# Performance work log

Hardware: AMD Instinct MI355X
Metric: run time of the kernel (lower is better)

Reference implementation:

```python
import jax, jax.numpy as jnp
import numpy as np

B, T, D, U = 32, 2048, 512, 512

def setup_inputs() -> dict:
    key = jax.random.key(0)
    ks = jax.random.split(key, 8)
    s = 0.02
    return {
        "query": jax.random.normal(ks[0], (B, D), dtype=jnp.float32),
        "values": jax.random.normal(ks[1], (B, T, D), dtype=jnp.float32),
        "W1_w": jax.random.normal(ks[2], (D, U), dtype=jnp.float32) * s,
        "W1_b": jnp.zeros((U,), dtype=jnp.float32),
        "W2_w": jax.random.normal(ks[3], (D, U), dtype=jnp.float32) * s,
        "W2_b": jnp.zeros((U,), dtype=jnp.float32),
        "V_w": jax.random.normal(ks[4], (U, 1), dtype=jnp.float32) * s,
        "V_b": jnp.zeros((1,), dtype=jnp.float32),
    }

def reference(query, values, W1_w, W1_b, W2_w, W2_b, V_w, V_b):
    # query: [B, D] -> [B, 1, U]; values: [B, T, D] -> [B, T, U]
    q_proj = (query @ W1_w + W1_b)[:, None, :]              # [B, 1, U]
    v_proj = jnp.einsum('btd,du->btu', values, W2_w) + W2_b  # [B, T, U]
    score = jnp.tanh(q_proj + v_proj) @ V_w + V_b            # [B, T, 1]
    attn = jax.nn.softmax(score, axis=1)                     # [B, T, 1]
    context = jnp.sum(attn * values, axis=1)                 # [B, D]
    return context, attn
```

## Files before the change

### kernel.cpp

```cpp
#include <hip/hip_runtime.h>
#include <hip/hip_bf16.h>
#include <cstddef>
#include <cstdint>

#define B_ 32
#define T_ 2048
#define D_ 512
#define U_ 512

typedef __attribute__((ext_vector_type(8))) short bf16x8;
typedef __attribute__((ext_vector_type(4))) float f32x4;

__device__ __forceinline__ unsigned short f2bf(float f) {
  union { float f; unsigned u; } x; x.f = f;
  unsigned r = x.u + 0x7fffu + ((x.u >> 16) & 1u);
  return (unsigned short)(r >> 16);
}
__device__ __forceinline__ unsigned pack2bf(float a, float b) {
  return (unsigned)f2bf(a) | ((unsigned)f2bf(b) << 16);
}
__device__ __forceinline__ float tanh_fast(float x) {
  float e = __expf(2.0f * x);
  return 1.0f - 2.0f * __builtin_amdgcn_rcpf(e + 1.0f);
}

#define AS1C(p) ((const __attribute__((address_space(1))) unsigned*)(p))
#define AS3(p)  ((__attribute__((address_space(3))) unsigned*)(p))

__global__ void kA_prep(const float* __restrict__ W2, unsigned* __restrict__ W2P,
                        const float* __restrict__ query, const float* __restrict__ W1,
                        const float* __restrict__ W1b, const float* __restrict__ W2b,
                        float* __restrict__ qp, float* __restrict__ score,
                        float* __restrict__ ctx) {
  const int tid = threadIdx.x;
  if (blockIdx.x < 256) {
    #pragma unroll
    for (int ii = 0; ii < 2; ++ii) {
      int p = blockIdx.x * 512 + ii * 256 + tid;
      int j = (p & 3) * 2;
      int l = (p >> 2) & 63;
      int t = p >> 8;
      int u = (t >> 4) * 16 + (l & 15);
      int k = (t & 15) * 32 + ((l >> 4) << 3) + j;
      W2P[p] = pack2bf(W2[(size_t)k * U_ + u], W2[(size_t)(k + 1) * U_ + u]);
    }
  } else {
    __shared__ float qs[D_];
    const int blk = blockIdx.x - 256;
    const int b = blk >> 1, uhh = (blk & 1) * 256;
    qs[tid] = query[b * D_ + tid];
    qs[tid + 256] = query[b * D_ + tid + 256];
    __syncthreads();
    const int u = uhh + tid;
    float a0 = 0, a1 = 0, a2 = 0, a3 = 0, a4 = 0, a5 = 0, a6 = 0, a7 = 0;
    for (int d = 0; d < D_; d += 8) {
      a0 += qs[d + 0] * W1[(size_t)(d + 0) * U_ + u];
      a1 += qs[d + 1] * W1[(size_t)(d + 1) * U_ + u];
      a2 += qs[d + 2] * W1[(size_t)(d + 2) * U_ + u];
      a3 += qs[d + 3] * W1[(size_t)(d + 3) * U_ + u];
      a4 += qs[d + 4] * W1[(size_t)(d + 4) * U_ + u];
      a5 += qs[d + 5] * W1[(size_t)(d + 5) * U_ + u];
      a6 += qs[d + 6] * W1[(size_t)(d + 6) * U_ + u];
      a7 += qs[d + 7] * W1[(size_t)(d + 7) * U_ + u];
    }
    qp[b * U_ + u] = ((a0 + a1) + (a2 + a3)) + ((a4 + a5) + (a6 + a7)) + W1b[u] + W2b[u];
    const int gt = blk * 256 + tid;
    ctx[gt] = 0.0f;
    #pragma unroll
    for (int i = 0; i < 4; ++i) score[i * 16384 + gt] = 0.0f;
  }
}

__global__ __launch_bounds__(256, 3) void k2_dma(
    const float* __restrict__ values, const unsigned short* __restrict__ W2P,
    const float* __restrict__ qp, const float* __restrict__ Vw,
    float* __restrict__ score) {
  __shared__ float av[2][4096];
  const int tid = threadIdx.x;
  const int bx = blockIdx.x;
  const int mt = bx >> 1, uh = bx & 1;
  const int m0 = mt * 64;
  const int b = m0 >> 11;
  const int l = tid & 63, w = tid >> 6;
  const int lr = l & 15, lq = l >> 4;

  const int drow = l >> 4;
  const int dchunk = l & 15;

  f32x4 acc[4][4];
  #pragma unroll
  for (int mi = 0; mi < 4; ++mi)
    #pragma unroll
    for (int ni = 0; ni < 4; ++ni) acc[mi][ni] = (f32x4){0.f, 0.f, 0.f, 0.f};

  const unsigned short* Bb = W2P + (size_t)(uh * 16 + w * 4) * 8192 + (size_t)l * 8;

  auto stage = [&](int e, int p) {
    #pragma unroll
    for (int j = 0; j < 4; ++j) {
      int g = w * 4 + j;
      int row = g * 4 + drow;
      int q = dchunk ^ (row & 15);
      const float* gp = values + (size_t)(m0 + row) * D_ + e * 64 + q * 4;
      __builtin_amdgcn_global_load_lds(AS1C(gp), AS3(&av[p][g * 256]), 16, 0, 0);
    }
  };

  bf16x8 Bc[4], Bn[4];
  stage(0, 0);
  #pragma unroll
  for (int ni = 0; ni < 4; ++ni) Bc[ni] = *(const bf16x8*)(Bb + (size_t)ni * 8192);

  for (int kg = 0; kg < 16; ++kg) {
    const int e = kg >> 1, p = e & 1;
    if ((kg & 1) == 0) {
      __syncthreads();
      if (e < 7) stage(e + 1, p ^ 1);
    }
    if (kg < 15) {
      #pragma unroll
      for (int ni = 0; ni < 4; ++ni)
        Bn[ni] = *(const bf16x8*)(Bb + (size_t)ni * 8192 + (size_t)(kg + 1) * 512);
    }
    const int kq = kg & 1;
    bf16x8 a[4];
    #pragma unroll
    for (int mi = 0; mi < 4; ++mi) {
      const int row = mi * 16 + lr;
      const int p0 = (kq * 8 + lq * 2) ^ lr;
      f32x4 flo = *(const f32x4*)&av[p][row * 64 + (p0 << 2)];
      f32x4 fhi = *(const f32x4*)&av[p][row * 64 + ((p0 ^ 1) << 2)];
      union { bf16x8 v; __hip_bfloat162 h[4]; } A;
      A.h[0] = __float22bfloat162_rn(make_float2(flo.x, flo.y));
      A.h[1] = __float22bfloat162_rn(make_float2(flo.z, flo.w));
      A.h[2] = __float22bfloat162_rn(make_float2(fhi.x, fhi.y));
      A.h[3] = __float22bfloat162_rn(make_float2(fhi.z, fhi.w));
      a[mi] = A.v;
    }
    #pragma unroll
    for (int ni = 0; ni < 4; ++ni)
      #pragma unroll
      for (int mi = 0; mi < 4; ++mi)
        acc[mi][ni] = __builtin_amdgcn_mfma_f32_16x16x32_bf16(a[mi], Bc[ni], acc[mi][ni], 0, 0, 0);
    #pragma unroll
    for (int ni = 0; ni < 4; ++ni) Bc[ni] = Bn[ni];
  }

  float sacc[4][4];
  #pragma unroll
  for (int mi = 0; mi < 4; ++mi)
    #pragma unroll
    for (int r = 0; r < 4; ++r) sacc[mi][r] = 0.0f;
  #pragma unroll
  for (int ni = 0; ni < 4; ++ni) {
    int u = uh * 256 + w * 64 + ni * 16 + lr;
    float qpv = qp[b * U_ + u], vv = Vw[u];
    #pragma unroll
    for (int mi = 0; mi < 4; ++mi)
      #pragma unroll
      for (int r = 0; r < 4; ++r)
        sacc[mi][r] += tanh_fast(acc[mi][ni][r] + qpv) * vv;
  }
  #pragma unroll
  for (int mi = 0; mi < 4; ++mi)
    #pragma unroll
    for (int r = 0; r < 4; ++r) {
      float v = sacc[mi][r];
      v += __shfl_xor(v, 1); v += __shfl_xor(v, 2);
      v += __shfl_xor(v, 4); v += __shfl_xor(v, 8);
      if (lr == 0) atomicAdd(&score[m0 + mi * 16 + lq * 4 + r], v);
    }
}

__global__ void k3_softmax(const float* __restrict__ score, float* __restrict__ attn) {
  __shared__ float red[8];
  const int b = blockIdx.x, tid = threadIdx.x;
  const float* s = score + b * T_;
  float v[8];
  float mx = -1e30f;
  #pragma unroll
  for (int i = 0; i < 8; ++i) { v[i] = s[tid + i * 256]; mx = fmaxf(mx, v[i]); }
  #pragma unroll
  for (int off = 1; off < 64; off <<= 1) mx = fmaxf(mx, __shfl_xor(mx, off));
  if ((tid & 63) == 0) red[tid >> 6] = mx;
  __syncthreads();
  mx = fmaxf(fmaxf(red[0], red[1]), fmaxf(red[2], red[3]));
  float sum = 0.0f;
  #pragma unroll
  for (int i = 0; i < 8; ++i) { v[i] = __expf(v[i] - mx); sum += v[i]; }
  #pragma unroll
  for (int off = 1; off < 64; off <<= 1) sum += __shfl_xor(sum, off);
  if ((tid & 63) == 0) red[4 + (tid >> 6)] = sum;
  __syncthreads();
  sum = (red[4] + red[5]) + (red[6] + red[7]);
  float inv = 1.0f / sum;
  #pragma unroll
  for (int i = 0; i < 8; ++i) attn[b * T_ + tid + i * 256] = v[i] * inv;
}

__global__ void k4_ctx(const float* __restrict__ values, const float* __restrict__ attn,
                       float* __restrict__ ctx) {
  __shared__ float at[64];
  __shared__ float ps[512];
  const int blk = blockIdx.x;
  const int b = blk >> 5, tc = blk & 31;
  const int tid = threadIdx.x;
  if (tid < 64) at[tid] = attn[b * T_ + tc * 64 + tid];
  __syncthreads();
  const int q = tid & 127;
  const int r0 = tid >> 7;
  const float4* vb = (const float4*)(values + ((size_t)b * T_ + tc * 64) * D_);
  float ax = 0.f, ay = 0.f, az = 0.f, aw = 0.f;
  #pragma unroll 8
  for (int tt = 0; tt < 32; ++tt) {
    int row = tt * 2 + r0;
    float4 v = vb[(size_t)row * 128 + q];
    float a = at[row];
    ax += a * v.x; ay += a * v.y; az += a * v.z; aw += a * v.w;
  }
  if (r0 == 1) { ps[4 * q] = ax; ps[4 * q + 1] = ay; ps[4 * q + 2] = az; ps[4 * q + 3] = aw; }
  __syncthreads();
  if (r0 == 0) {
    atomicAdd(&ctx[b * D_ + 4 * q + 0], ax + ps[4 * q + 0]);
    atomicAdd(&ctx[b * D_ + 4 * q + 1], ay + ps[4 * q + 1]);
    atomicAdd(&ctx[b * D_ + 4 * q + 2], az + ps[4 * q + 2]);
    atomicAdd(&ctx[b * D_ + 4 * q + 3], aw + ps[4 * q + 3]);
  }
}

extern "C" void kernel_launch(void* const* d_in, const int* in_sizes, int n_in,
                              void* d_out, int out_size, void* d_ws, size_t ws_size,
                              hipStream_t stream) {
  const float* query = (const float*)d_in[0];
  const float* values = (const float*)d_in[1];
  const float* W1w = (const float*)d_in[2];
  const float* W1b = (const float*)d_in[3];
  const float* W2w = (const float*)d_in[4];
  const float* W2b = (const float*)d_in[5];
  const float* Vw  = (const float*)d_in[6];

  float* out = (float*)d_out;
  float* ctx  = out;
  float* attn = out + B_ * D_;
  float* score = attn;

  char* ws = (char*)d_ws;
  unsigned* W2P = (unsigned*)ws;
  float* qp    = (float*)(ws + 512 * 1024);

  kA_prep<<<320, 256, 0, stream>>>(W2w, W2P, query, W1w, W1b, W2b, qp, score, ctx);
  k2_dma<<<2048, 256, 0, stream>>>(values, (const unsigned short*)W2P, qp, Vw, score);
  k3_softmax<<<32, 256, 0, stream>>>(score, attn);
  k4_ctx<<<1024, 256, 0, stream>>>(values, attn, ctx);
}
```

Baseline: 276.6 us.

## Deepen values pipeline to four LDS stages and coalesce W2 prepack via LDS transpose

The GEMM kernel now keeps four LDS buffers for the values tiles and stages two steps ahead, using explicit vmcnt waits and raw s_barrier in place of __syncthreads. It also loads W2 fragments for a whole 64-wide chunk in double-buffered registers and raises MFMA priority with s_setprio. The W2 bf16 prepack is rewritten to read rows coalesced into shared memory and write the permuted layout from there, which cuts the prep grid from 320 to 80 blocks. The extra 64KB of LDS drops occupancy from 3 to 2 blocks per CU, and the hand-counted vmcnt values depend on the exact number of outstanding loads.

```diff
diff --git a/kernel.cpp b/kernel.cpp
--- a/kernel.cpp
+++ b/kernel.cpp
@@ -15,9 +15,6 @@
   union { float f; unsigned u; } x; x.f = f;
   unsigned r = x.u + 0x7fffu + ((x.u >> 16) & 1u);
   return (unsigned short)(r >> 16);
-}
-__device__ __forceinline__ unsigned pack2bf(float a, float b) {
-  return (unsigned)f2bf(a) | ((unsigned)f2bf(b) << 16);
 }
 __device__ __forceinline__ float tanh_fast(float x) {
   float e = __expf(2.0f * x);
@@ -33,20 +30,28 @@
                         float* __restrict__ qp, float* __restrict__ score,
                         float* __restrict__ ctx) {
   const int tid = threadIdx.x;
-  if (blockIdx.x < 256) {
-    #pragma unroll
-    for (int ii = 0; ii < 2; ++ii) {
-      int p = blockIdx.x * 512 + ii * 256 + tid;
-      int j = (p & 3) * 2;
-      int l = (p >> 2) & 63;
-      int t = p >> 8;
-      int u = (t >> 4) * 16 + (l & 15);
-      int k = (t & 15) * 32 + ((l >> 4) << 3) + j;
-      W2P[p] = pack2bf(W2[(size_t)k * U_ + u], W2[(size_t)(k + 1) * U_ + u]);
-    }
+  if (blockIdx.x < 16) {
+    const int kg = blockIdx.x;
+    __shared__ unsigned short w2s[32][514];
+    const float4* W2v = (const float4*)(W2 + (size_t)kg * 32 * U_);
+    #pragma unroll
+    for (int i = 0; i < 16; ++i) {
+      int idx = i * 256 + tid;
+      float4 v = W2v[idx];
+      int r = idx >> 7, c = (idx & 127) * 4;
+      w2s[r][c + 0] = f2bf(v.x); w2s[r][c + 1] = f2bf(v.y);
+      w2s[r][c + 2] = f2bf(v.z); w2s[r][c + 3] = f2bf(v.w);
+    }
+    __syncthreads();
+    const int lq = tid >> 6, lr = (tid >> 2) & 15, j = tid & 3;
+    const int kb = lq * 8 + j * 2;
+    #pragma unroll
+    for (int ut = 0; ut < 32; ++ut)
+      W2P[ut * 4096 + kg * 256 + tid] =
+          (unsigned)w2s[kb][ut * 16 + lr] | ((unsigned)w2s[kb + 1][ut * 16 + lr] << 16);
   } else {
     __shared__ float qs[D_];
-    const int blk = blockIdx.x - 256;
+    const int blk = blockIdx.x - 16;
     const int b = blk >> 1, uhh = (blk & 1) * 256;
     qs[tid] = query[b * D_ + tid];
     qs[tid + 256] = query[b * D_ + tid + 256];
@@ -71,11 +76,11 @@
   }
 }
 
-__global__ __launch_bounds__(256, 3) void k2_dma(
+__global__ __launch_bounds__(256, 2) void k2_dma(
     const float* __restrict__ values, const unsigned short* __restrict__ W2P,
     const float* __restrict__ qp, const float* __restrict__ Vw,
     float* __restrict__ score) {
-  __shared__ float av[2][4096];
+  __shared__ float av[4][4096];
   const int tid = threadIdx.x;
   const int bx = blockIdx.x;
   const int mt = bx >> 1, uh = bx & 1;
@@ -95,55 +100,69 @@
 
   const unsigned short* Bb = W2P + (size_t)(uh * 16 + w * 4) * 8192 + (size_t)l * 8;
 
-  auto stage = [&](int e, int p) {
+  auto stage = [&](int s) {
+    const int p = s & 3;
     #pragma unroll
     for (int j = 0; j < 4; ++j) {
       int g = w * 4 + j;
       int row = g * 4 + drow;
       int q = dchunk ^ (row & 15);
-      const float* gp = values + (size_t)(m0 + row) * D_ + e * 64 + q * 4;
+      const float* gp = values + (size_t)(m0 + row) * D_ + s * 64 + q * 4;
       __builtin_amdgcn_global_load_lds(AS1C(gp), AS3(&av[p][g * 256]), 16, 0, 0);
     }
   };
 
-  bf16x8 Bc[4], Bn[4];
-  stage(0, 0);
-  #pragma unroll
-  for (int ni = 0; ni < 4; ++ni) Bc[ni] = *(const bf16x8*)(Bb + (size_t)ni * 8192);
-
-  for (int kg = 0; kg < 16; ++kg) {
-    const int e = kg >> 1, p = e & 1;
-    if ((kg & 1) == 0) {
-      __syncthreads();
-      if (e < 7) stage(e + 1, p ^ 1);
-    }
-    if (kg < 15) {
+  bf16x8 Bf[2][8];
+  auto loadB = [&](int ph) {
+    const int slot = ph & 1;
+    #pragma unroll
+    for (int kq = 0; kq < 2; ++kq)
       #pragma unroll
       for (int ni = 0; ni < 4; ++ni)
-        Bn[ni] = *(const bf16x8*)(Bb + (size_t)ni * 8192 + (size_t)(kg + 1) * 512);
-    }
-    const int kq = kg & 1;
-    bf16x8 a[4];
-    #pragma unroll
-    for (int mi = 0; mi < 4; ++mi) {
-      const int row = mi * 16 + lr;
-      const int p0 = (kq * 8 + lq * 2) ^ lr;
-      f32x4 flo = *(const f32x4*)&av[p][row * 64 + (p0 << 2)];
-      f32x4 fhi = *(const f32x4*)&av[p][row * 64 + ((p0 ^ 1) << 2)];
-      union { bf16x8 v; __hip_bfloat162 h[4]; } A;
-      A.h[0] = __float22bfloat162_rn(make_float2(flo.x, flo.y));
-      A.h[1] = __float22bfloat162_rn(make_float2(flo.z, flo.w));
-      A.h[2] = __float22bfloat162_rn(make_float2(fhi.x, fhi.y));
-      A.h[3] = __float22bfloat162_rn(make_float2(fhi.z, fhi.w));
-      a[mi] = A.v;
-    }
-    #pragma unroll
-    for (int ni = 0; ni < 4; ++ni)
-      #pragma unroll
-      for (int mi = 0; mi < 4; ++mi)
-        acc[mi][ni] = __builtin_amdgcn_mfma_f32_16x16x32_bf16(a[mi], Bc[ni], acc[mi][ni], 0, 0, 0);
-    #pragma unroll
-    for (int ni = 0; ni < 4; ++ni) Bc[ni] = Bn[ni];
+        Bf[slot][kq * 4 + ni] =
+            *(const bf16x8*)(Bb + (size_t)ni * 8192 + (size_t)(2 * ph + kq) * 512);
+  };
+
+  loadB(0);
+  stage(0);
+  loadB(1);
+  stage(1);
+
+  #pragma unroll
+  for (int e = 0; e < 8; ++e) {
+    __builtin_amdgcn_sched_barrier(0);
+    if (e == 7) asm volatile("s_waitcnt vmcnt(8)" ::: "memory");
+    else        asm volatile("s_waitcnt vmcnt(12)" ::: "memory");
+    __builtin_amdgcn_s_barrier();
+    __builtin_amdgcn_sched_barrier(0);
+    if (e < 7) loadB(e + 1);
+    if (e < 6) stage(e + 2);
+
+    #pragma unroll
+    for (int kq = 0; kq < 2; ++kq) {
+      bf16x8 a[4];
+      #pragma unroll
+      for (int mi = 0; mi < 4; ++mi) {
+        const int row = mi * 16 + lr;
+        const int p0 = (kq * 8 + lq * 2) ^ lr;
+        f32x4 flo = *(const f32x4*)&av[e & 3][row * 64 + (p0 << 2)];
+        f32x4 fhi = *(const f32x4*)&av[e & 3][row * 64 + ((p0 ^ 1) << 2)];
+        union { bf16x8 v; __hip_bfloat162 h[4]; } A;
+        A.h[0] = __float22bfloat162_rn(make_float2(flo.x, flo.y));
+        A.h[1] = __float22bfloat162_rn(make_float2(flo.z, flo.w));
+        A.h[2] = __float22bfloat162_rn(make_float2(fhi.x, fhi.y));
+        A.h[3] = __float22bfloat162_rn(make_float2(fhi.z, fhi.w));
+        a[mi] = A.v;
+      }
+      __builtin_amdgcn_s_setprio(1);
+      #pragma unroll
+      for (int ni = 0; ni < 4; ++ni)
+        #pragma unroll
+        for (int mi = 0; mi < 4; ++mi)
+          acc[mi][ni] = __builtin_amdgcn_mfma_f32_16x16x32_bf16(
+              a[mi], Bf[e & 1][kq * 4 + ni], acc[mi][ni], 0, 0, 0);
+      __builtin_amdgcn_s_setprio(0);
+    }
   }
 
   float sacc[4][4];
@@ -248,7 +267,7 @@
   unsigned* W2P = (unsigned*)ws;
   float* qp    = (float*)(ws + 512 * 1024);
 
-  kA_prep<<<320, 256, 0, stream>>>(W2w, W2P, query, W1w, W1b, W2b, qp, score, ctx);
+  kA_prep<<<80, 256, 0, stream>>>(W2w, W2P, query, W1w, W1b, W2b, qp, score, ctx);
   k2_dma<<<2048, 256, 0, stream>>>(values, (const unsigned short*)W2P, qp, Vw, score);
   k3_softmax<<<32, 256, 0, stream>>>(score, attn);
   k4_ctx<<<1024, 256, 0, stream>>>(values, attn, ctx);
```

Result: no change. 279.2 us (+0.9%).
